# Performance work log

Measured on AMD Instinct MI355X. Metric: run time of the kernel, lower is better.

## Reference

```python
import jax, jax.numpy as jnp
import numpy as np
from jax import lax

D_MODEL = 512
D_STATE = 16
D_CONV = 4
EXPAND = 2
D_INNER = EXPAND * D_MODEL          # 1024
DT_RANK = (D_MODEL + 15) // 16      # 32 (ceil(d_model/16))
BATCH = 8
SEQLEN = 2048


def _mamba_params(key):
    ks = jax.random.split(key, 6)
    s = 0.02
    return {
        'in_w':   jax.random.normal(ks[0], (2 * D_INNER, D_MODEL)) * s,
        'conv_w': jax.random.normal(ks[1], (D_INNER, D_CONV)) * s,
        'conv_b': jnp.zeros((D_INNER,)),
        'xp_w':   jax.random.normal(ks[2], (DT_RANK + 2 * D_STATE, D_INNER)) * s,
        'dt_w':   jax.random.normal(ks[3], (D_INNER, DT_RANK)) * s,
        'dt_b':   jax.random.uniform(ks[4], (D_INNER,), minval=-4.0, maxval=-2.0),
        'A_log':  jnp.log(jnp.tile(jnp.arange(1, D_STATE + 1, dtype=jnp.float32), (D_INNER, 1))),
        'Dp':     jnp.ones((D_INNER,)),
        'out_w':  jax.random.normal(ks[5], (D_MODEL, D_INNER)) * s,
    }


def setup_inputs() -> dict:
    key = jax.random.key(0)
    kx, kf, kb, kl1, kl2 = jax.random.split(key, 5)
    pf = _mamba_params(kf)
    pb = _mamba_params(kb)
    inp = {'x': jax.random.normal(kx, (BATCH, SEQLEN, D_MODEL), dtype=jnp.float32)}
    for name, v in pf.items():
        inp['f_' + name] = v
    for name, v in pb.items():
        inp['b_' + name] = v
    inp['lin_w'] = jax.random.normal(kl1, (D_MODEL, 2 * D_MODEL)) * 0.02
    inp['lin_b'] = jnp.zeros((D_MODEL,))
    return inp


def _mamba(x, in_w, conv_w, conv_b, xp_w, dt_w, dt_b, A_log, Dp, out_w):
    # x: (B, L, D_MODEL)
    Bsz = x.shape[0]
    xz = x @ in_w.T                                  # (B, L, 2*D_INNER)
    xi, z = jnp.split(xz, 2, axis=-1)
    # causal depthwise conv over time
    xc = jnp.transpose(xi, (0, 2, 1))                # (B, D_INNER, L)
    xc = lax.conv_general_dilated(
        xc, conv_w[:, None, :], (1,), [(D_CONV - 1, 0)],
        feature_group_count=D_INNER)
    xi = jax.nn.silu(jnp.transpose(xc + conv_b[None, :, None], (0, 2, 1)))
    # input-dependent SSM params
    dbl = xi @ xp_w.T                                # (B, L, DT_RANK + 2*N)
    dt = jax.nn.softplus(dbl[..., :DT_RANK] @ dt_w.T + dt_b)    # (B, L, D_INNER)
    Bm = dbl[..., DT_RANK:DT_RANK + D_STATE]                    # (B, L, N)
    Cm = dbl[..., DT_RANK + D_STATE:]                           # (B, L, N)
    A = -jnp.exp(A_log)                                         # (D_INNER, N)

    def step(h, inp):
        dt_t, B_t, C_t, x_t = inp                    # (B,Di), (B,N), (B,N), (B,Di)
        h = jnp.exp(dt_t[..., None] * A) * h + (dt_t * x_t)[..., None] * B_t[:, None, :]
        y = jnp.einsum('bdn,bn->bd', h, C_t)
        return h, y

    xs = (jnp.swapaxes(dt, 0, 1), jnp.swapaxes(Bm, 0, 1),
          jnp.swapaxes(Cm, 0, 1), jnp.swapaxes(xi, 0, 1))
    h0 = jnp.zeros((Bsz, D_INNER, D_STATE), dtype=x.dtype)
    _, ys = lax.scan(step, h0, xs)                   # ys: (L, B, D_INNER)
    y = jnp.swapaxes(ys, 0, 1) + xi * Dp
    y = y * jax.nn.silu(z)
    return y @ out_w.T                               # (B, L, D_MODEL)


def reference(x,
              f_in_w, f_conv_w, f_conv_b, f_xp_w, f_dt_w, f_dt_b, f_A_log, f_Dp, f_out_w,
              b_in_w, b_conv_w, b_conv_b, b_xp_w, b_dt_w, b_dt_b, b_A_log, b_Dp, b_out_w,
              lin_w, lin_b):
    y_fwd = _mamba(x, f_in_w, f_conv_w, f_conv_b, f_xp_w, f_dt_w, f_dt_b, f_A_log, f_Dp, f_out_w)
    y_bwd = _mamba(x[:, ::-1, :], b_in_w, b_conv_w, b_conv_b, b_xp_w, b_dt_w, b_dt_b,
                   b_A_log, b_Dp, b_out_w)[:, ::-1, :]
    y = jnp.concatenate([y_fwd, y_bwd], axis=-1)     # (B, L, 2*D_MODEL)
    return y @ lin_w.T + lin_b
```

## Files before the change

### kernel.cpp

```cpp
#include <hip/hip_runtime.h>
#include <cmath>

#define LSEQ 2048
#define NBATCH 8

typedef __attribute__((ext_vector_type(8))) short short8;
typedef __attribute__((ext_vector_type(4))) float f32x4;
typedef __attribute__((ext_vector_type(2))) float f32x2;

__device__ __forceinline__ float silu_f(float x) {
    return x * __builtin_amdgcn_rcpf(1.0f + __expf(-x));
}
__device__ __forceinline__ float softplus_f(float x) {
    return fmaxf(x, 0.0f) + __logf(1.0f + __expf(-fabsf(x)));
}
__device__ __forceinline__ unsigned short f2bf(float f) {
    unsigned int u = __float_as_uint(f);
    u += 0x7FFFu + ((u >> 16) & 1u);
    return (unsigned short)(u >> 16);
}
__device__ __forceinline__ float bf2f(unsigned short h) {
    return __uint_as_float(((unsigned int)h) << 16);
}
__device__ __forceinline__ void gload_lds16(const void* g, void* l) {
    __builtin_amdgcn_global_load_lds((const __attribute__((address_space(1))) void*)g,
                                     (__attribute__((address_space(3))) void*)l, 16, 0, 0);
}

#if defined(__has_builtin)
#if __has_builtin(__builtin_amdgcn_exp2f)
#define EXP2F(x) __builtin_amdgcn_exp2f(x)
#endif
#endif
#ifndef EXP2F
#define EXP2F(x) __expf((x) * 0.69314718055994531f)
#endif

struct GemmPair {
    const unsigned short* A[2];
    const unsigned short* A2[2];
    const unsigned short* W[2];
    const float* bias[2];
    void* C[2];
    void* Cz[2];
    unsigned short* aux[2];
};

template<int WGM, int WGN, int OMODE, int DK, int XTRA, int SPLIT = 0>
__global__ __launch_bounds__(WGM* WGN * 64) void gemm_mfma(GemmPair gp, int lda, int ldw,
                                                           int ldc, int K)
{
    constexpr int NW = WGM * WGN;
    constexpr int TM = WGM * 64, TN = WGN * 64;
    __shared__ unsigned short As[TM * 32];
    __shared__ unsigned short Bs[TN * 32];
    const int dir = blockIdx.z;
    const unsigned short* A  = gp.A[dir];
    const unsigned short* A2 = gp.A2[dir];
    const unsigned short* W  = gp.W[dir];
    const float* bias        = gp.bias[dir];
    void* Cout               = gp.C[dir];
    void* Czout              = gp.Cz[dir];
    unsigned short* aux      = gp.aux[dir];

    const int tid = threadIdx.x;
    const int wave = tid >> 6, lane = tid & 63;
    const int wm = wave / WGN, wn = wave % WGN;
    const int m0 = blockIdx.x * TM, n0 = blockIdx.y * TN;
    const int l15 = lane & 15, l4 = lane >> 4;
    const int srow = lane >> 2, schunk = (lane & 3) * 8;

    f32x4 acc[4][4] = {};

    for (int k0 = 0; k0 < K; k0 += 32) {
        __syncthreads();
        for (int s = wave; s < TM / 16; s += NW) {
            const int gr = m0 + s * 16 + srow;
            const unsigned short* g;
            if (DK != 0 && k0 >= DK)
                g = A2 + (size_t)(gr ^ (LSEQ - 1)) * lda + (k0 - DK) + schunk;
            else
                g = A + (size_t)gr * lda + k0 + schunk;
            gload_lds16(g, (char*)As + (size_t)s * 1024);
        }
        for (int s = wave; s < TN / 16; s += NW) {
            const int gr = n0 + s * 16 + srow;
            const unsigned short* g = W + (size_t)gr * ldw + k0 + schunk;
            gload_lds16(g, (char*)Bs + (size_t)s * 1024);
        }
        __syncthreads();
        short8 af[4], bfr[4];
#pragma unroll
        for (int mi = 0; mi < 4; ++mi)
            af[mi] = *(const short8*)&As[(wm * 64 + mi * 16 + l15) * 32 + l4 * 8];
#pragma unroll
        for (int ni = 0; ni < 4; ++ni)
            bfr[ni] = *(const short8*)&Bs[(wn * 64 + ni * 16 + l15) * 32 + l4 * 8];
#pragma unroll
        for (int mi = 0; mi < 4; ++mi)
#pragma unroll
            for (int ni = 0; ni < 4; ++ni)
                acc[mi][ni] = __builtin_amdgcn_mfma_f32_16x16x32_bf16(af[mi], bfr[ni], acc[mi][ni], 0, 0, 0);
    }

    void* Cb = (SPLIT && blockIdx.y * TN >= 1024) ? Czout : Cout;
#pragma unroll
    for (int mi = 0; mi < 4; ++mi)
#pragma unroll
        for (int ni = 0; ni < 4; ++ni)
#pragma unroll
            for (int r = 0; r < 4; ++r) {
                const int row = m0 + wm * 64 + mi * 16 + l4 * 4 + r;
                const int col = n0 + wn * 64 + ni * 16 + l15;
                const int colL = SPLIT ? (col & 1023) : col;
                float v = acc[mi][ni][r];
                if (bias) v += bias[col];
                if (OMODE & 1) ((unsigned short*)Cb)[(size_t)row * ldc + colL] = f2bf(v);
                else           ((float*)Cb)[(size_t)row * ldc + colL] = v;
                if (XTRA) { if (col < 32) aux[(size_t)row * 32 + col] = f2bf(v); }
            }
}

__global__ __launch_bounds__(256) void combine_k(
    const float* __restrict__ lin_w, const float* __restrict__ owf,
    const float* __restrict__ owb, unsigned short* __restrict__ Wcomb)
{
    const int dir = blockIdx.z;
    const float* ow = dir ? owb : owf;
    const int lane = threadIdx.x & 63;
    const int wave = threadIdx.x >> 6;
    const int n = blockIdx.y * 4 + wave;
    const int d = blockIdx.x * 256 + lane * 4;
    float4 acc = {0.f, 0.f, 0.f, 0.f};
    const float* lrow = lin_w + (size_t)n * 1024 + dir * 512;
    for (int j = 0; j < 512; ++j) {
        const float s = lrow[j];
        const float4 v = *(const float4*)&ow[(size_t)j * 1024 + d];
        acc.x = fmaf(s, v.x, acc.x); acc.y = fmaf(s, v.y, acc.y);
        acc.z = fmaf(s, v.z, acc.z); acc.w = fmaf(s, v.w, acc.w);
    }
    ushort4 o;
    o.x = f2bf(acc.x); o.y = f2bf(acc.y); o.z = f2bf(acc.z); o.w = f2bf(acc.w);
    *(ushort4*)&Wcomb[(size_t)n * 2048 + dir * 1024 + d] = o;
}

struct CvtArgs { const float* s[6]; unsigned short* d[6]; int n[6]; };
__global__ __launch_bounds__(256) void cvt_k(CvtArgs a)
{
    const int sid = blockIdx.y;
    const float* s = a.s[sid];
    unsigned short* d = a.d[sid];
    const int n4 = a.n[sid] >> 2;
    for (int i = blockIdx.x * 256 + threadIdx.x; i < n4; i += gridDim.x * 256) {
        const float4 v = ((const float4*)s)[i];
        ushort4 o; o.x = f2bf(v.x); o.y = f2bf(v.y); o.z = f2bf(v.z); o.w = f2bf(v.w);
        ((ushort4*)d)[i] = o;
    }
}
__global__ __launch_bounds__(256) void cvtx_k(const float* __restrict__ s,
                                              unsigned short* __restrict__ d, int n4)
{
    for (int i = blockIdx.x * 256 + threadIdx.x; i < n4; i += gridDim.x * 256) {
        const float4 v = ((const float4*)s)[i];
        ushort4 o; o.x = f2bf(v.x); o.y = f2bf(v.y); o.z = f2bf(v.z); o.w = f2bf(v.w);
        ((ushort4*)d)[i] = o;
    }
}

__global__ __launch_bounds__(256) void alprep_k(const float* __restrict__ af,
                                                const float* __restrict__ ab,
                                                float* __restrict__ of,
                                                float* __restrict__ ob)
{
    const int i = blockIdx.x * 256 + threadIdx.x;
    if (i < 16384) {
        of[i] = -expf(af[i]) * 1.4426950408889634f;
        ob[i] = -expf(ab[i]) * 1.4426950408889634f;
    }
}

__global__ __launch_bounds__(256) void conv_silu_k(
    const unsigned short* __restrict__ xc_f, const float* __restrict__ cw_f,
    const float* __restrict__ cb_f, unsigned short* __restrict__ xi_f,
    const unsigned short* __restrict__ xc_b, const float* __restrict__ cw_b,
    const float* __restrict__ cb_b, unsigned short* __restrict__ xi_b)
{
    const int dir = blockIdx.y;
    const unsigned short* xc = dir ? xc_b : xc_f;
    const float* cw = dir ? cw_b : cw_f;
    const float* cb = dir ? cb_b : cb_f;
    unsigned short* xi = dir ? xi_b : xi_f;

    const int bt = blockIdx.x;
    const int b = bt >> 8;
    const int t0 = (bt & 255) << 3;
    const int d = threadIdx.x << 2;

    float w[4][4];
#pragma unroll
    for (int i = 0; i < 4; ++i) {
        const float4 wr = *(const float4*)&cw[(d + i) * 4];
        w[i][0] = wr.x; w[i][1] = wr.y; w[i][2] = wr.z; w[i][3] = wr.w;
    }
    const float4 bias = *(const float4*)&cb[d];

    float4 r[11];
#pragma unroll
    for (int j = 0; j < 11; ++j) {
        const int row = dir ? (LSEQ + 2 - t0 - j) : (t0 - 3 + j);
        if ((unsigned)row < (unsigned)LSEQ) {
            const ushort4 v = *(const ushort4*)&xc[(size_t)(b * LSEQ + row) * 1024 + d];
            r[j].x = bf2f(v.x); r[j].y = bf2f(v.y); r[j].z = bf2f(v.z); r[j].w = bf2f(v.w);
        } else {
            r[j].x = 0.f; r[j].y = 0.f; r[j].z = 0.f; r[j].w = 0.f;
        }
    }
#pragma unroll
    for (int tt = 0; tt < 8; ++tt) {
        float4 acc = bias;
#pragma unroll
        for (int k = 0; k < 4; ++k) {
            const float4 v = r[tt + k];
            acc.x += w[0][k] * v.x; acc.y += w[1][k] * v.y;
            acc.z += w[2][k] * v.z; acc.w += w[3][k] * v.w;
        }
        ushort4 st;
        st.x = f2bf(silu_f(acc.x)); st.y = f2bf(silu_f(acc.y));
        st.z = f2bf(silu_f(acc.z)); st.w = f2bf(silu_f(acc.w));
        *(ushort4*)&xi[(size_t)(b * LSEQ + t0 + tt) * 1024 + d] = st;
    }
}

__device__ __forceinline__ float row_sum8(float x) {
    x += __int_as_float(__builtin_amdgcn_update_dpp(0, __float_as_int(x), 0xB1, 0xF, 0xF, true));
    x += __int_as_float(__builtin_amdgcn_update_dpp(0, __float_as_int(x), 0x4E, 0xF, 0xF, true));
    x += __int_as_float(__builtin_amdgcn_update_dpp(0, __float_as_int(x), 0x141, 0xF, 0xF, true));
    return x;
}

struct ScanPair {
    const unsigned short* dblh[2];
    const unsigned short* dtw[2];
    const float* dtb[2];
    unsigned short* xiy[2];
    const float* dbl[2];
    const unsigned short* zb[2];
    const float* Al[2];
    const float* Dp[2];
    float* cumg[2];
    float* he[2];
};

__global__ __launch_bounds__(256, 4) void scan_k(ScanPair sp)
{
    __shared__ unsigned short sxi[64][40];
    __shared__ float sdt[32][68], sdtx[32][68];
    __shared__ float sB2[8][140], sC2[8][140];
    __shared__ float sy[32][66];

    const int dir = blockIdx.z;
    const unsigned short* dblh = sp.dblh[dir];
    const unsigned short* dtw  = sp.dtw[dir];
    const float* dtb           = sp.dtb[dir];
    unsigned short* xiy        = sp.xiy[dir];
    const float* dbl           = sp.dbl[dir];
    const unsigned short* zz   = sp.zb[dir];
    const float* Al            = sp.Al[dir];
    const float* Dpp           = sp.Dp[dir];
    float* cumg                = sp.cumg[dir];
    float* hep                 = sp.he[dir];

    const int by = blockIdx.y;
    const int b = by >> 1, part = by & 1;
    const int rbase = b * LSEQ + part * (LSEQ / 2);
    const int d0 = blockIdx.x << 5;
    const int tid = threadIdx.x;
    const int wave = tid >> 6, lane = tid & 63;
    const int l15 = lane & 15, l4 = lane >> 4;
    const int di = tid >> 3, np = tid & 7;
    const int lr = tid >> 2, lc = tid & 3;
    const bool lead = (np == 0);

    const f32x2 ALv = {-expf(Al[(d0 + di) * 16 + np]) * 1.4426950408889634f,
                       -expf(Al[(d0 + di) * 16 + np + 8]) * 1.4426950408889634f};

    const short8 dtwf0 = *(const short8*)&dtw[(size_t)(d0 + l15) * 32 + l4 * 8];
    const short8 dtwf1 = *(const short8*)&dtw[(size_t)(d0 + 16 + l15) * 32 + l4 * 8];
    const float dtb0 = dtb[d0 + l15], dtb1 = dtb[d0 + 16 + l15];

    float dpv[8];
#pragma unroll
    for (int i = 0; i < 8; ++i) dpv[i] = Dpp[d0 + lc * 8 + i];

    ushort4 pxi0, pxi1;
    float4 pB, pC;
    short8 pA;
    auto issue_loads = [&](int c) {
        const size_t r = (size_t)rbase + c * 64 + lr;
        pxi0 = *(const ushort4*)&xiy[r * 1024 + d0 + lc * 8];
        pxi1 = *(const ushort4*)&xiy[r * 1024 + d0 + lc * 8 + 4];
        pB   = *(const float4*)&dbl[r * 64 + 32 + lc * 4];
        pC   = *(const float4*)&dbl[r * 64 + 48 + lc * 4];
        pA   = *(const short8*)&dblh[(size_t)(rbase + c * 64 + wave * 16 + l15) * 32 + l4 * 8];
    };
    issue_loads(0);

    constexpr int NT = (LSEQ / 2) / 64;
    f32x2 h = {0.f, 0.f};
    float cum = 0.0f;
    for (int c = 0; c < NT; ++c) {
        const int t0 = c * 64;
        *(ushort4*)&sxi[lr][lc * 8]     = pxi0;
        *(ushort4*)&sxi[lr][lc * 8 + 4] = pxi1;
        {
            const float bv[4] = {pB.x, pB.y, pB.z, pB.w};
            const float cv[4] = {pC.x, pC.y, pC.z, pC.w};
#pragma unroll
            for (int i = 0; i < 4; ++i) {
                const int n = lc * 4 + i;
                sB2[n & 7][lr * 2 + (n >> 3)] = bv[i];
                sC2[n & 7][lr * 2 + (n >> 3)] = cv[i];
            }
        }
        if (part) __syncthreads();
        {
            f32x4 z4 = {0.f, 0.f, 0.f, 0.f};
            f32x4 dacc0 = __builtin_amdgcn_mfma_f32_16x16x32_bf16(pA, dtwf0, z4, 0, 0, 0);
            f32x4 dacc1 = __builtin_amdgcn_mfma_f32_16x16x32_bf16(pA, dtwf1, z4, 0, 0, 0);
            const int tq = wave * 16 + l4 * 4;
            float4 xi0, xi1;
            xi0.x = bf2f(sxi[tq + 0][l15]);      xi0.y = bf2f(sxi[tq + 1][l15]);
            xi0.z = bf2f(sxi[tq + 2][l15]);      xi0.w = bf2f(sxi[tq + 3][l15]);
            xi1.x = bf2f(sxi[tq + 0][16 + l15]); xi1.y = bf2f(sxi[tq + 1][16 + l15]);
            xi1.z = bf2f(sxi[tq + 2][16 + l15]); xi1.w = bf2f(sxi[tq + 3][16 + l15]);
            float4 dv0, dv1, dx0, dx1;
            dv0.x = softplus_f(dacc0[0] + dtb0); dv0.y = softplus_f(dacc0[1] + dtb0);
            dv0.z = softplus_f(dacc0[2] + dtb0); dv0.w = softplus_f(dacc0[3] + dtb0);
            dv1.x = softplus_f(dacc1[0] + dtb1); dv1.y = softplus_f(dacc1[1] + dtb1);
            dv1.z = softplus_f(dacc1[2] + dtb1); dv1.w = softplus_f(dacc1[3] + dtb1);
            dx0.x = dv0.x * xi0.x; dx0.y = dv0.y * xi0.y;
            dx0.z = dv0.z * xi0.z; dx0.w = dv0.w * xi0.w;
            dx1.x = dv1.x * xi1.x; dx1.y = dv1.y * xi1.y;
            dx1.z = dv1.z * xi1.z; dx1.w = dv1.w * xi1.w;
            *(float4*)&sdt[l15][tq]       = dv0;
            *(float4*)&sdt[16 + l15][tq]  = dv1;
            *(float4*)&sdtx[l15][tq]      = dx0;
            *(float4*)&sdtx[16 + l15][tq] = dx1;
        }
        const ushort4 oxi0 = pxi0, oxi1 = pxi1;
        ushort4 pz0 = {}, pz1 = {};
        if (part == 0) {
            const int tg = t0 + lr;
            const int tz = dir ? (LSEQ - 1 - tg) : tg;
            pz0 = *(const ushort4*)&zz[((size_t)b * LSEQ + tz) * 1024 + d0 + lc * 8];
            pz1 = *(const ushort4*)&zz[((size_t)b * LSEQ + tz) * 1024 + d0 + lc * 8 + 4];
        }
        if (c + 1 < NT) issue_loads(c + 1);
        __syncthreads();
#pragma unroll 4
        for (int tt = 0; tt < 64; tt += 4) {
            const float4 d4 = *(const float4*)&sdt[di][tt];
            const float4 u4 = *(const float4*)&sdtx[di][tt];
            const float4 bA = *(const float4*)&sB2[np][tt * 2];
            const float4 bB = *(const float4*)&sB2[np][tt * 2 + 4];
            const float4 cA = *(const float4*)&sC2[np][tt * 2];
            const float4 cB = *(const float4*)&sC2[np][tt * 2 + 4];
            float4 ppv;
            {
                f32x2 e = ALv * d4.x;
                e.x = EXP2F(e.x); e.y = EXP2F(e.y);
                const f32x2 b2 = {bA.x, bA.y};
                const f32x2 c2 = {cA.x, cA.y};
                h = e * h + b2 * u4.x;
                const f32x2 pc = h * c2;
                ppv.x = row_sum8(pc.x + pc.y);
            }
            {
                f32x2 e = ALv * d4.y;
                e.x = EXP2F(e.x); e.y = EXP2F(e.y);
                const f32x2 b2 = {bA.z, bA.w};
                const f32x2 c2 = {cA.z, cA.w};
                h = e * h + b2 * u4.y;
                const f32x2 pc = h * c2;
                ppv.y = row_sum8(pc.x + pc.y);
            }
            {
                f32x2 e = ALv * d4.z;
                e.x = EXP2F(e.x); e.y = EXP2F(e.y);
                const f32x2 b2 = {bB.x, bB.y};
                const f32x2 c2 = {cB.x, cB.y};
                h = e * h + b2 * u4.z;
                const f32x2 pc = h * c2;
                ppv.z = row_sum8(pc.x + pc.y);
            }
            {
                f32x2 e = ALv * d4.w;
                e.x = EXP2F(e.x); e.y = EXP2F(e.y);
                const f32x2 b2 = {bB.z, bB.w};
                const f32x2 c2 = {cB.z, cB.w};
                h = e * h + b2 * u4.w;
                const f32x2 pc = h * c2;
                ppv.w = row_sum8(pc.x + pc.y);
            }
            if (part) {
                const float c0 = cum + d4.x, c1 = c0 + d4.y;
                const float c2s = c1 + d4.z, c3 = c2s + d4.w;
                cum = c3;
                if (lead) {
                    float4 cc; cc.x = c0; cc.y = c1; cc.z = c2s; cc.w = c3;
                    *(float4*)&sdt[di][tt] = cc;
                }
            }
            if (lead) *(float4*)&sy[di][tt] = ppv;
        }
        __syncthreads();
        if (part == 0) {
            const size_t r = (size_t)rbase + t0 + lr;
            ushort4 s0, s1;
            s0.x = f2bf(fmaf(bf2f(oxi0.x), dpv[0], sy[lc * 8 + 0][lr]) * silu_f(bf2f(pz0.x)));
            s0.y = f2bf(fmaf(bf2f(oxi0.y), dpv[1], sy[lc * 8 + 1][lr]) * silu_f(bf2f(pz0.y)));
            s0.z = f2bf(fmaf(bf2f(oxi0.z), dpv[2], sy[lc * 8 + 2][lr]) * silu_f(bf2f(pz0.z)));
            s0.w = f2bf(fmaf(bf2f(oxi0.w), dpv[3], sy[lc * 8 + 3][lr]) * silu_f(bf2f(pz0.w)));
            s1.x = f2bf(fmaf(bf2f(oxi1.x), dpv[4], sy[lc * 8 + 4][lr]) * silu_f(bf2f(pz1.x)));
            s1.y = f2bf(fmaf(bf2f(oxi1.y), dpv[5], sy[lc * 8 + 5][lr]) * silu_f(bf2f(pz1.y)));
            s1.z = f2bf(fmaf(bf2f(oxi1.z), dpv[6], sy[lc * 8 + 6][lr]) * silu_f(bf2f(pz1.z)));
            s1.w = f2bf(fmaf(bf2f(oxi1.w), dpv[7], sy[lc * 8 + 7][lr]) * silu_f(bf2f(pz1.w)));
            *(ushort4*)&xiy[r * 1024 + d0 + lc * 8] = s0;
            *(ushort4*)&xiy[r * 1024 + d0 + lc * 8 + 4] = s1;
        } else {
            const size_t r = (size_t)rbase + t0 + lr;
            ushort4 s0, s1;
            s0.x = f2bf(fmaf(bf2f(oxi0.x), dpv[0], sy[lc * 8 + 0][lr]));
            s0.y = f2bf(fmaf(bf2f(oxi0.y), dpv[1], sy[lc * 8 + 1][lr]));
            s0.z = f2bf(fmaf(bf2f(oxi0.z), dpv[2], sy[lc * 8 + 2][lr]));
            s0.w = f2bf(fmaf(bf2f(oxi0.w), dpv[3], sy[lc * 8 + 3][lr]));
            s1.x = f2bf(fmaf(bf2f(oxi1.x), dpv[4], sy[lc * 8 + 4][lr]));
            s1.y = f2bf(fmaf(bf2f(oxi1.y), dpv[5], sy[lc * 8 + 5][lr]));
            s1.z = f2bf(fmaf(bf2f(oxi1.z), dpv[6], sy[lc * 8 + 6][lr]));
            s1.w = f2bf(fmaf(bf2f(oxi1.w), dpv[7], sy[lc * 8 + 7][lr]));
            *(ushort4*)&xiy[r * 1024 + d0 + lc * 8] = s0;
            *(ushort4*)&xiy[r * 1024 + d0 + lc * 8 + 4] = s1;
            float4 c0v, c1v;
            c0v.x = sdt[lc * 8 + 0][lr]; c0v.y = sdt[lc * 8 + 1][lr];
            c0v.z = sdt[lc * 8 + 2][lr]; c0v.w = sdt[lc * 8 + 3][lr];
            c1v.x = sdt[lc * 8 + 4][lr]; c1v.y = sdt[lc * 8 + 5][lr];
            c1v.z = sdt[lc * 8 + 6][lr]; c1v.w = sdt[lc * 8 + 7][lr];
            const size_t pr = (size_t)(b * (LSEQ / 2) + t0 + lr) * 1024 + d0 + lc * 8;
            *(float4*)&cumg[pr]     = c0v;
            *(float4*)&cumg[pr + 4] = c1v;
        }
    }
    if (part == 0) {
        float* hh = &hep[((size_t)b * 1024 + d0 + di) * 16 + np];
        hh[0] = h.x; hh[8] = h.y;
    }
}

struct FixArgs {
    const float* cumg[2]; const float* he[2]; const float* al2[2];
    const float* dbl[2];  const unsigned short* zb[2]; unsigned short* xiy[2];
};
__global__ __launch_bounds__(256) void fix_k(FixArgs a)
{
    const int dir = blockIdx.z;
    const float* cumg          = a.cumg[dir];
    const float* he            = a.he[dir];
    const float* al2           = a.al2[dir];
    const float* dbl           = a.dbl[dir];
    const unsigned short* zz   = a.zb[dir];
    unsigned short* xiy        = a.xiy[dir];

    __shared__ float sAL[32][17], sHE[32][17];
    __shared__ float sCt[256][16];

    const int tid = threadIdx.x;
    const int d0 = blockIdx.x << 5;
    const int by = blockIdx.y;
    const int b = by >> 2, q = by & 3;
    const int tq0 = q << 8;

    for (int i = tid; i < 512; i += 256) {
        const int dd = i >> 4, nn = i & 15;
        sAL[dd][nn] = al2[(size_t)(d0 + dd) * 16 + nn];
        sHE[dd][nn] = he[((size_t)b * 1024 + d0 + dd) * 16 + nn];
    }
    for (int i = tid; i < 4096; i += 256) {
        const int tt = i >> 4, nn = i & 15;
        sCt[tt][nn] = dbl[((size_t)b * LSEQ + (LSEQ / 2) + tq0 + tt) * 64 + 48 + nn];
    }
    __syncthreads();

    const int ts = tid >> 4, dd = (tid & 15) * 2;
    for (int it = 0; it < 16; ++it) {
        const int tloc = it * 16 + ts;
        const int tl = tq0 + tloc;
        const int tglob = (LSEQ / 2) + tl;
        const size_t grow = (size_t)b * LSEQ + tglob;
        const float2 cv = *(const float2*)&cumg[((size_t)b * (LSEQ / 2) + tl) * 1024 + d0 + dd];
        const ushort2 yv = *(const ushort2*)&xiy[grow * 1024 + d0 + dd];
        const int tz = dir ? (LSEQ - 1 - tglob) : tglob;
        const ushort2 zv = *(const ushort2*)&zz[((size_t)b * LSEQ + tz) * 1024 + d0 + dd];
        float corr0 = 0.f, corr1 = 0.f;
#pragma unroll
        for (int n = 0; n < 16; ++n) {
            const float ct = sCt[tloc][n];
            corr0 = fmaf(ct * sHE[dd + 0][n], EXP2F(sAL[dd + 0][n] * cv.x), corr0);
            corr1 = fmaf(ct * sHE[dd + 1][n], EXP2F(sAL[dd + 1][n] * cv.y), corr1);
        }
        ushort2 o;
        o.x = f2bf((bf2f(yv.x) + corr0) * silu_f(bf2f(zv.x)));
        o.y = f2bf((bf2f(yv.y) + corr1) * silu_f(bf2f(zv.y)));
        *(ushort2*)&xiy[grow * 1024 + d0 + dd] = o;
    }
}

extern "C" void kernel_launch(void* const* d_in, const int* in_sizes, int n_in,
                              void* d_out, int out_size, void* d_ws, size_t ws_size,
                              hipStream_t stream)
{
    const float* x      = (const float*)d_in[0];
    const float* f_in_w = (const float*)d_in[1];
    const float* f_cw   = (const float*)d_in[2];
    const float* f_cb   = (const float*)d_in[3];
    const float* f_xp   = (const float*)d_in[4];
    const float* f_dtw  = (const float*)d_in[5];
    const float* f_dtb  = (const float*)d_in[6];
    const float* f_Al   = (const float*)d_in[7];
    const float* f_Dp   = (const float*)d_in[8];
    const float* f_ow   = (const float*)d_in[9];
    const float* b_in_w = (const float*)d_in[10];
    const float* b_cw   = (const float*)d_in[11];
    const float* b_cb   = (const float*)d_in[12];
    const float* b_xp   = (const float*)d_in[13];
    const float* b_dtw  = (const float*)d_in[14];
    const float* b_dtb  = (const float*)d_in[15];
    const float* b_Al   = (const float*)d_in[16];
    const float* b_Dp   = (const float*)d_in[17];
    const float* b_ow   = (const float*)d_in[18];
    const float* lin_w  = (const float*)d_in[19];
    const float* lin_b  = (const float*)d_in[20];
    float* out = (float*)d_out;

    char* p = (char*)d_ws;
    auto take = [&](size_t bytes) -> char* {
        char* r = p; p += (bytes + 255) & ~(size_t)255; return r;
    };

    unsigned short* wif  = (unsigned short*)take((size_t)2048 * 512 * 2);
    unsigned short* wib  = (unsigned short*)take((size_t)2048 * 512 * 2);
    unsigned short* wxf  = (unsigned short*)take((size_t)64 * 1024 * 2);
    unsigned short* wxb  = (unsigned short*)take((size_t)64 * 1024 * 2);
    unsigned short* wdtf = (unsigned short*)take((size_t)1024 * 32 * 2);
    unsigned short* wdtb = (unsigned short*)take((size_t)1024 * 32 * 2);
    unsigned short* wcmb = (unsigned short*)take((size_t)512 * 2048 * 2);
    float* al2f = (float*)take((size_t)1024 * 16 * 4);
    float* al2b = (float*)take((size_t)1024 * 16 * 4);

    const size_t used = (size_t)(p - (char*)d_ws);
    const size_t perRow = 1024 + 2 * (2048 + 2048 + 2048 + 256 + 64);
    int G = 1;
    for (int g = 8; g >= 1; g >>= 1) {
        const size_t need = used + (size_t)g * LSEQ * perRow + (size_t)g * 2 * 1024 * 16 * 4 + 16384;
        if (need <= ws_size || g == 1) { G = g; break; }
    }

    CvtArgs ca;
    ca.s[0] = f_in_w; ca.d[0] = wif;  ca.n[0] = 2048 * 512;
    ca.s[1] = b_in_w; ca.d[1] = wib;  ca.n[1] = 2048 * 512;
    ca.s[2] = f_xp;   ca.d[2] = wxf;  ca.n[2] = 64 * 1024;
    ca.s[3] = b_xp;   ca.d[3] = wxb;  ca.n[3] = 64 * 1024;
    ca.s[4] = f_dtw;  ca.d[4] = wdtf; ca.n[4] = 1024 * 32;
    ca.s[5] = b_dtw;  ca.d[5] = wdtb; ca.n[5] = 1024 * 32;
    cvt_k<<<dim3(128, 6), 256, 0, stream>>>(ca);

    alprep_k<<<dim3(64), 256, 0, stream>>>(f_Al, b_Al, al2f, al2b);

    combine_k<<<dim3(4, 128, 2), 256, 0, stream>>>(lin_w, f_ow, b_ow, wcmb);

    char* pg0 = p;
    for (int g0 = 0; g0 < NBATCH; g0 += G) {
        const int Mg = G * LSEQ;
        p = pg0;
        unsigned short* xbf   = (unsigned short*)take((size_t)Mg * 512 * 2);
        unsigned short* xc_f  = (unsigned short*)take((size_t)Mg * 1024 * 2);
        unsigned short* zb_f  = (unsigned short*)take((size_t)Mg * 1024 * 2);
        unsigned short* xc_b  = (unsigned short*)take((size_t)Mg * 1024 * 2);
        unsigned short* zb_b  = (unsigned short*)take((size_t)Mg * 1024 * 2);
        unsigned short* xiy_f = (unsigned short*)take((size_t)Mg * 1024 * 2);
        unsigned short* xiy_b = (unsigned short*)take((size_t)Mg * 1024 * 2);
        float* dbl_f          = (float*)take((size_t)Mg * 64 * 4);
        float* dbl_b          = (float*)take((size_t)Mg * 64 * 4);
        unsigned short* dblh_f= (unsigned short*)take((size_t)Mg * 32 * 2);
        unsigned short* dblh_b= (unsigned short*)take((size_t)Mg * 32 * 2);
        float* he_f           = (float*)take((size_t)G * 1024 * 16 * 4);
        float* he_b           = (float*)take((size_t)G * 1024 * 16 * 4);
        float* cum_f = (float*)xc_f;
        float* cum_b = (float*)xc_b;

        const float* xg = x + (size_t)g0 * LSEQ * 512;
        float* outg = out + (size_t)g0 * LSEQ * 512;

        cvtx_k<<<dim3(512), 256, 0, stream>>>(xg, xbf, Mg * 512 / 4);

        GemmPair g1 = {};
        g1.A[0] = xbf; g1.A[1] = xbf; g1.W[0] = wif; g1.W[1] = wib;
        g1.C[0] = xc_f; g1.C[1] = xc_b; g1.Cz[0] = zb_f; g1.Cz[1] = zb_b;
        gemm_mfma<2,2,1,0,0,1><<<dim3(Mg/128, 16, 2), 256, 0, stream>>>(g1, 512, 512, 1024, 512);

        conv_silu_k<<<dim3(Mg/8, 2), 256, 0, stream>>>(xc_f, f_cw, f_cb, xiy_f,
                                                       xc_b, b_cw, b_cb, xiy_b);

        GemmPair g2 = {};
        g2.A[0] = xiy_f; g2.A[1] = xiy_b; g2.W[0] = wxf; g2.W[1] = wxb;
        g2.C[0] = dbl_f; g2.C[1] = dbl_b; g2.aux[0] = dblh_f; g2.aux[1] = dblh_b;
        gemm_mfma<2,1,0,0,1><<<dim3(Mg/128, 1, 2), 128, 0, stream>>>(g2, 1024, 1024, 64, 1024);

        ScanPair spp = {};
        spp.dblh[0] = dblh_f; spp.dblh[1] = dblh_b;
        spp.dtw[0] = wdtf;    spp.dtw[1] = wdtb;
        spp.dtb[0] = f_dtb;   spp.dtb[1] = b_dtb;
        spp.xiy[0] = xiy_f;   spp.xiy[1] = xiy_b;
        spp.dbl[0] = dbl_f;   spp.dbl[1] = dbl_b;
        spp.zb[0] = zb_f;     spp.zb[1] = zb_b;
        spp.Al[0] = f_Al;     spp.Al[1] = b_Al;
        spp.Dp[0] = f_Dp;     spp.Dp[1] = b_Dp;
        spp.cumg[0] = cum_f;  spp.cumg[1] = cum_b;
        spp.he[0] = he_f;     spp.he[1] = he_b;
        scan_k<<<dim3(32, G * 2, 2), 256, 0, stream>>>(spp);

        FixArgs fa = {};
        fa.cumg[0] = cum_f; fa.cumg[1] = cum_b;
        fa.he[0] = he_f;    fa.he[1] = he_b;
        fa.al2[0] = al2f;   fa.al2[1] = al2b;
        fa.dbl[0] = dbl_f;  fa.dbl[1] = dbl_b;
        fa.zb[0] = zb_f;    fa.zb[1] = zb_b;
        fa.xiy[0] = xiy_f;  fa.xiy[1] = xiy_b;
        fix_k<<<dim3(32, G * 4, 2), 256, 0, stream>>>(fa);

        GemmPair g5 = {};
        g5.A[0] = xiy_f; g5.A2[0] = xiy_b; g5.W[0] = wcmb;
        g5.bias[0] = lin_b; g5.C[0] = outg;
        gemm_mfma<2,2,0,1024,0><<<dim3(Mg/128, 4, 1), 256, 0, stream>>>(g5, 1024, 2048, 512, 2048);
    }
}
```

Measured before the change: 661.7 us.

## Exploit structured A_log in fix kernel, widen conv tile, fuse scan C-dot

Adds a runtime check that A_log rows follow A[n] = (n+1)*A[0]. When they do, fix_k replaces 16 exp2 calls per element with one exp2 followed by repeated multiplication. Separately, conv_silu_k now handles 16 timesteps per block instead of 8, which cuts redundant halo loads. The scan's C-dot product is rewritten as a fused fma. The power-chain path relies on a property of the test's A_log initialisation and may accumulate slightly more rounding error, but it falls back to the original path when the check fails.

```diff
diff --git a/kernel.cpp b/kernel.cpp
--- a/kernel.cpp
+++ b/kernel.cpp
@@ -144,9 +144,10 @@
     *(ushort4*)&Wcomb[(size_t)n * 2048 + dir * 1024 + d] = o;
 }
 
-struct CvtArgs { const float* s[6]; unsigned short* d[6]; int n[6]; };
+struct CvtArgs { const float* s[6]; unsigned short* d[6]; int n[6]; int* flag; };
 __global__ __launch_bounds__(256) void cvt_k(CvtArgs a)
 {
+    if (blockIdx.x == 0 && blockIdx.y == 0 && threadIdx.x == 0) *a.flag = 0;
     const int sid = blockIdx.y;
     const float* s = a.s[sid];
     unsigned short* d = a.d[sid];
@@ -170,12 +171,22 @@
 __global__ __launch_bounds__(256) void alprep_k(const float* __restrict__ af,
                                                 const float* __restrict__ ab,
                                                 float* __restrict__ of,
-                                                float* __restrict__ ob)
+                                                float* __restrict__ ob,
+                                                int* __restrict__ flag)
 {
     const int i = blockIdx.x * 256 + threadIdx.x;
     if (i < 16384) {
-        of[i] = -expf(af[i]) * 1.4426950408889634f;
-        ob[i] = -expf(ab[i]) * 1.4426950408889634f;
+        const float vf = -expf(af[i]) * 1.4426950408889634f;
+        const float vb = -expf(ab[i]) * 1.4426950408889634f;
+        of[i] = vf;
+        ob[i] = vb;
+        const int n = i & 15, d0i = i & ~15;
+        const float k = (float)(n + 1);
+        const float uf = -expf(af[d0i]) * 1.4426950408889634f;
+        const float ub = -expf(ab[d0i]) * 1.4426950408889634f;
+        const bool devf = fabsf(vf - k * uf) > 1e-4f * fabsf(vf) + 1e-6f;
+        const bool devb = fabsf(vb - k * ub) > 1e-4f * fabsf(vb) + 1e-6f;
+        if (devf || devb) *flag = 1;
     }
 }
 
@@ -192,8 +203,8 @@
     unsigned short* xi = dir ? xi_b : xi_f;
 
     const int bt = blockIdx.x;
-    const int b = bt >> 8;
-    const int t0 = (bt & 255) << 3;
+    const int b = bt >> 7;
+    const int t0 = (bt & 127) << 4;
     const int d = threadIdx.x << 2;
 
     float w[4][4];
@@ -204,9 +215,9 @@
     }
     const float4 bias = *(const float4*)&cb[d];
 
-    float4 r[11];
-#pragma unroll
-    for (int j = 0; j < 11; ++j) {
+    float4 r[19];
+#pragma unroll
+    for (int j = 0; j < 19; ++j) {
         const int row = dir ? (LSEQ + 2 - t0 - j) : (t0 - 3 + j);
         if ((unsigned)row < (unsigned)LSEQ) {
             const ushort4 v = *(const ushort4*)&xc[(size_t)(b * LSEQ + row) * 1024 + d];
@@ -216,7 +227,7 @@
         }
     }
 #pragma unroll
-    for (int tt = 0; tt < 8; ++tt) {
+    for (int tt = 0; tt < 16; ++tt) {
         float4 acc = bias;
 #pragma unroll
         for (int k = 0; k < 4; ++k) {
@@ -370,37 +381,29 @@
                 f32x2 e = ALv * d4.x;
                 e.x = EXP2F(e.x); e.y = EXP2F(e.y);
                 const f32x2 b2 = {bA.x, bA.y};
-                const f32x2 c2 = {cA.x, cA.y};
                 h = e * h + b2 * u4.x;
-                const f32x2 pc = h * c2;
-                ppv.x = row_sum8(pc.x + pc.y);
+                ppv.x = row_sum8(fmaf(h.y, cA.y, h.x * cA.x));
             }
             {
                 f32x2 e = ALv * d4.y;
                 e.x = EXP2F(e.x); e.y = EXP2F(e.y);
                 const f32x2 b2 = {bA.z, bA.w};
-                const f32x2 c2 = {cA.z, cA.w};
                 h = e * h + b2 * u4.y;
-                const f32x2 pc = h * c2;
-                ppv.y = row_sum8(pc.x + pc.y);
+                ppv.y = row_sum8(fmaf(h.y, cA.w, h.x * cA.z));
             }
             {
                 f32x2 e = ALv * d4.z;
                 e.x = EXP2F(e.x); e.y = EXP2F(e.y);
                 const f32x2 b2 = {bB.x, bB.y};
-                const f32x2 c2 = {cB.x, cB.y};
                 h = e * h + b2 * u4.z;
-                const f32x2 pc = h * c2;
-                ppv.z = row_sum8(pc.x + pc.y);
+                ppv.z = row_sum8(fmaf(h.y, cB.y, h.x * cB.x));
             }
             {
                 f32x2 e = ALv * d4.w;
                 e.x = EXP2F(e.x); e.y = EXP2F(e.y);
                 const f32x2 b2 = {bB.z, bB.w};
-                const f32x2 c2 = {cB.z, cB.w};
                 h = e * h + b2 * u4.w;
-                const f32x2 pc = h * c2;
-                ppv.w = row_sum8(pc.x + pc.y);
+                ppv.w = row_sum8(fmaf(h.y, cB.w, h.x * cB.z));
             }
             if (part) {
                 const float c0 = cum + d4.x, c1 = c0 + d4.y;
@@ -459,6 +462,7 @@
 struct FixArgs {
     const float* cumg[2]; const float* he[2]; const float* al2[2];
     const float* dbl[2];  const unsigned short* zb[2]; unsigned short* xiy[2];
+    const int* flag;
 };
 __global__ __launch_bounds__(256) void fix_k(FixArgs a)
 {
@@ -469,6 +473,7 @@
     const float* dbl           = a.dbl[dir];
     const unsigned short* zz   = a.zb[dir];
     unsigned short* xiy        = a.xiy[dir];
+    const int notStruct        = *a.flag;
 
     __shared__ float sAL[32][17], sHE[32][17];
     __shared__ float sCt[256][16];
@@ -501,11 +506,24 @@
         const int tz = dir ? (LSEQ - 1 - tglob) : tglob;
         const ushort2 zv = *(const ushort2*)&zz[((size_t)b * LSEQ + tz) * 1024 + d0 + dd];
         float corr0 = 0.f, corr1 = 0.f;
-#pragma unroll
-        for (int n = 0; n < 16; ++n) {
-            const float ct = sCt[tloc][n];
-            corr0 = fmaf(ct * sHE[dd + 0][n], EXP2F(sAL[dd + 0][n] * cv.x), corr0);
-            corr1 = fmaf(ct * sHE[dd + 1][n], EXP2F(sAL[dd + 1][n] * cv.y), corr1);
+        if (!notStruct) {
+            const float E0 = EXP2F(sAL[dd + 0][0] * cv.x);
+            const float E1 = EXP2F(sAL[dd + 1][0] * cv.y);
+            float En0 = E0, En1 = E1;
+#pragma unroll
+            for (int n = 0; n < 16; ++n) {
+                const float ct = sCt[tloc][n];
+                corr0 = fmaf(ct * sHE[dd + 0][n], En0, corr0);
+                corr1 = fmaf(ct * sHE[dd + 1][n], En1, corr1);
+                En0 *= E0; En1 *= E1;
+            }
+        } else {
+#pragma unroll
+            for (int n = 0; n < 16; ++n) {
+                const float ct = sCt[tloc][n];
+                corr0 = fmaf(ct * sHE[dd + 0][n], EXP2F(sAL[dd + 0][n] * cv.x), corr0);
+                corr1 = fmaf(ct * sHE[dd + 1][n], EXP2F(sAL[dd + 1][n] * cv.y), corr1);
+            }
         }
         ushort2 o;
         o.x = f2bf((bf2f(yv.x) + corr0) * silu_f(bf2f(zv.x)));
@@ -555,6 +573,7 @@
     unsigned short* wcmb = (unsigned short*)take((size_t)512 * 2048 * 2);
     float* al2f = (float*)take((size_t)1024 * 16 * 4);
     float* al2b = (float*)take((size_t)1024 * 16 * 4);
+    int* sflag  = (int*)take(256);
 
     const size_t used = (size_t)(p - (char*)d_ws);
     const size_t perRow = 1024 + 2 * (2048 + 2048 + 2048 + 256 + 64);
@@ -571,9 +590,10 @@
     ca.s[3] = b_xp;   ca.d[3] = wxb;  ca.n[3] = 64 * 1024;
     ca.s[4] = f_dtw;  ca.d[4] = wdtf; ca.n[4] = 1024 * 32;
     ca.s[5] = b_dtw;  ca.d[5] = wdtb; ca.n[5] = 1024 * 32;
+    ca.flag = sflag;
     cvt_k<<<dim3(128, 6), 256, 0, stream>>>(ca);
 
-    alprep_k<<<dim3(64), 256, 0, stream>>>(f_Al, b_Al, al2f, al2b);
+    alprep_k<<<dim3(64), 256, 0, stream>>>(f_Al, b_Al, al2f, al2b, sflag);
 
     combine_k<<<dim3(4, 128, 2), 256, 0, stream>>>(lin_w, f_ow, b_ow, wcmb);
 
@@ -607,8 +627,8 @@
         g1.C[0] = xc_f; g1.C[1] = xc_b; g1.Cz[0] = zb_f; g1.Cz[1] = zb_b;
         gemm_mfma<2,2,1,0,0,1><<<dim3(Mg/128, 16, 2), 256, 0, stream>>>(g1, 512, 512, 1024, 512);
 
-        conv_silu_k<<<dim3(Mg/8, 2), 256, 0, stream>>>(xc_f, f_cw, f_cb, xiy_f,
-                                                       xc_b, b_cw, b_cb, xiy_b);
+        conv_silu_k<<<dim3(Mg/16, 2), 256, 0, stream>>>(xc_f, f_cw, f_cb, xiy_f,
+                                                        xc_b, b_cw, b_cb, xiy_b);
 
         GemmPair g2 = {};
         g2.A[0] = xiy_f; g2.A[1] = xiy_b; g2.W[0] = wxf; g2.W[1] = wxb;
@@ -635,6 +655,7 @@
         fa.dbl[0] = dbl_f;  fa.dbl[1] = dbl_b;
         fa.zb[0] = zb_f;    fa.zb[1] = zb_b;
         fa.xiy[0] = xiy_f;  fa.xiy[1] = xiy_b;
+        fa.flag = sflag;
         fix_k<<<dim3(32, G * 4, 2), 256, 0, stream>>>(fa);
 
         GemmPair g5 = {};
```

New measurement: 680.6 us. 2.9% more time.
